# Kernel tuning notes

Measured on AMD Instinct MI355X. Metric: run time of the kernel, lower is better.

## Reference

```python
import jax, jax.numpy as jnp
import numpy as np

B, D_IN, D_HID, D_OUT, N_EXP, K = 32768, 256, 512, 256, 16, 2


def setup_inputs() -> dict:
    key = jax.random.key(0)
    ks = jax.random.split(key, 5)
    s_in = 1.0 / np.sqrt(D_IN)
    s_hid = 1.0 / np.sqrt(D_HID)
    return {
        "x": jax.random.normal(ks[0], (B, D_IN), jnp.float32),
        "Wg": jax.random.normal(ks[1], (D_IN, N_EXP), jnp.float32) * s_in,
        "bg": jnp.zeros((N_EXP,), jnp.float32),
        "W1": jax.random.normal(ks[2], (N_EXP, D_IN, D_HID), jnp.float32) * s_in,
        "b1": jnp.zeros((N_EXP, D_HID), jnp.float32),
        "W2": jax.random.normal(ks[3], (N_EXP, D_HID, D_OUT), jnp.float32) * s_hid,
        "b2": jnp.zeros((N_EXP, D_OUT), jnp.float32),
    }


def reference(x, Wg, bg, W1, b1, W2, b2):
    # Gating: linear -> softmax -> top-k -> renormalize (inference path, no noise)
    logits = x @ Wg + bg                       # [B, E]
    probs = jax.nn.softmax(logits, axis=-1)
    top_w, top_idx = jax.lax.top_k(probs, K)   # [B, K]
    top_w = top_w / jnp.sum(top_w, axis=-1, keepdims=True)

    # Expert MLPs (evaluate all experts densely, then gather selected outputs;
    # same math as masked gather -> MLP -> weighted scatter-add)
    h = jax.nn.relu(jnp.einsum('bi,eih->beh', x, W1) + b1[None])  # [B, E, H]
    y_all = jnp.einsum('beh,eho->beo', h, W2) + b2[None]          # [B, E, O]

    y_sel = jnp.take_along_axis(y_all, top_idx[:, :, None], axis=1)  # [B, K, O]
    return jnp.sum(y_sel * top_w[:, :, None], axis=1)                # [B, O]
```

## Files before the change

### kernel.cpp

```cpp
#include <hip/hip_runtime.h>
#include <stdint.h>

#define BTOK 32768
#define DIN 256
#define DHID 512
#define DOUT 256
#define NEXP 16
#define BM 128
#define CH 32
#define NCH 16
#define SLOTS 96

typedef __attribute__((ext_vector_type(8))) short bf16x8;
typedef __attribute__((ext_vector_type(4))) float f32x4;

__device__ __forceinline__ unsigned short f2bf(float f){
  unsigned u = __builtin_bit_cast(unsigned, f);
  u = u + 0x7FFFu + ((u >> 16) & 1u);
  return (unsigned short)(u >> 16);
}
__device__ __forceinline__ float bf2f(unsigned short h){
  return __builtin_bit_cast(float, (unsigned)h << 16);
}
__device__ __forceinline__ void gload16(const void* g, void* l){
  __builtin_amdgcn_global_load_lds((const __attribute__((address_space(1))) unsigned int*)g,
                                   (__attribute__((address_space(3))) unsigned int*)l, 16, 0, 0);
}

__global__ __launch_bounds__(256) void transpose_cvt(const float* __restrict__ src,
                                                     unsigned short* __restrict__ dst,
                                                     int R, int C){
  __shared__ float t[32][33];
  int e = blockIdx.z, r0 = blockIdx.y * 32, c0 = blockIdx.x * 32;
  int lx = threadIdx.x & 31, ly = threadIdx.x >> 5;
  const float* s = src + (size_t)e * R * C;
  unsigned short* d = dst + (size_t)e * R * C;
#pragma unroll
  for (int i = 0; i < 4; i++){ int r = ly + i * 8; t[r][lx] = s[(size_t)(r0 + r) * C + c0 + lx]; }
  __syncthreads();
#pragma unroll
  for (int i = 0; i < 4; i++){ int r = ly + i * 8; d[(size_t)(c0 + r) * R + r0 + lx] = f2bf(t[lx][r]); }
}

__global__ __launch_bounds__(256) void transpose_cvt_w2(const float* __restrict__ src,
                                                        unsigned short* __restrict__ dst){
  __shared__ float t[32][33];
  int e = blockIdx.z, r0 = blockIdx.y * 32, c0 = blockIdx.x * 32;
  int lx = threadIdx.x & 31, ly = threadIdx.x >> 5;
  const float* s = src + (size_t)e * DHID * DOUT;
  unsigned short* d = dst + (size_t)e * DHID * DOUT + (r0 >> 5) * (DOUT * CH);
#pragma unroll
  for (int i = 0; i < 4; i++){ int r = ly + i * 8; t[r][lx] = s[(size_t)(r0 + r) * DOUT + c0 + lx]; }
  __syncthreads();
#pragma unroll
  for (int i = 0; i < 4; i++){ int rr = ly + i * 8; d[(size_t)(c0 + rr) * CH + lx] = f2bf(t[lx][rr]); }
}

__global__ __launch_bounds__(256) void gating_kernel(const float* __restrict__ x,
                                                     const float* __restrict__ Wg,
                                                     const float* __restrict__ bg,
                                                     unsigned short* __restrict__ x_bf,
                                                     int* __restrict__ top_idx,
                                                     float* __restrict__ top_w,
                                                     int* __restrict__ counts){
  __shared__ float WgT[16][256];
  __shared__ int hist[16];
  int tid = threadIdx.x;
#pragma unroll
  for (int j = 0; j < 4; j++){
    float4 wv = *(const float4*)(Wg + tid * 16 + j * 4);
    WgT[j * 4 + 0][tid] = wv.x; WgT[j * 4 + 1][tid] = wv.y;
    WgT[j * 4 + 2][tid] = wv.z; WgT[j * 4 + 3][tid] = wv.w;
  }
  if (tid < 16) hist[tid] = 0;
  __syncthreads();
  int wid = tid >> 6, lane = tid & 63;

  for (int t = 0; t < 16; t++){
    int tok = blockIdx.x * 64 + wid * 16 + t;
    const float4 xv = *(const float4*)(x + (size_t)tok * DIN + lane * 4);
    ushort4 xb; xb.x = f2bf(xv.x); xb.y = f2bf(xv.y); xb.z = f2bf(xv.z); xb.w = f2bf(xv.w);
    *(ushort4*)(x_bf + (size_t)tok * DIN + lane * 4) = xb;
    float logit[16];
#pragma unroll
    for (int e = 0; e < 16; e++){
      const float4 wv = *(const float4*)(&WgT[e][lane * 4]);
      float v = xv.x * wv.x + xv.y * wv.y + xv.z * wv.z + xv.w * wv.w;
#pragma unroll
      for (int off = 32; off; off >>= 1) v += __shfl_xor(v, off, 64);
      logit[e] = v + bg[e];
    }
    if (lane == 0){
      int i1 = 0; float v1 = logit[0];
#pragma unroll
      for (int e = 1; e < 16; e++) if (logit[e] > v1){ v1 = logit[e]; i1 = e; }
      int i2 = -1; float v2 = -3.4e38f;
#pragma unroll
      for (int e = 0; e < 16; e++) if (e != i1 && logit[e] > v2){ v2 = logit[e]; i2 = e; }
      float tt = expf(v2 - v1);
      float w1 = 1.0f / (1.0f + tt);
      float w2 = tt / (1.0f + tt);
      top_idx[tok * 2] = i1; top_idx[tok * 2 + 1] = i2;
      top_w[tok * 2] = w1;  top_w[tok * 2 + 1] = w2;
      atomicAdd(&hist[i1], 1); atomicAdd(&hist[i2], 1);
    }
  }
  __syncthreads();
  if (tid < 16) atomicAdd(&counts[tid], hist[tid]);
}

__global__ void prefix_kernel(const int* __restrict__ counts, int* __restrict__ offsets,
                              int* __restrict__ cursor, int* __restrict__ bm_e,
                              int* __restrict__ bm_start, int* __restrict__ bm_end){
  int lane = threadIdx.x & 63;
  int c = (lane < 16) ? counts[lane] : 0;
  int s = c;
#pragma unroll
  for (int off = 1; off < 16; off <<= 1){ int o = __shfl_up(s, off, 64); if (lane >= off) s += o; }
  int start = s - c;
  if (lane < 16){ offsets[lane] = start; cursor[lane] = start; }
  int nb = (c + BM - 1) >> 7;
  int nb_partner = __shfl(nb, lane ^ 8, 64);
  if (lane < 8){
    int filled = nb + nb_partner;
    if (filled > SLOTS) filled = SLOTS;
    for (int i = filled; i < SLOTS; i++) bm_e[lane * SLOTS + i] = -1;
  }
  if (lane < 16){
    int sbase = (lane < 8) ? 0 : nb_partner;
    int xcd = lane & 7;
    for (int b = 0; b < nb; b++){
      int idx = xcd * SLOTS + sbase + b;
      if (sbase + b < SLOTS){
        bm_e[idx] = lane; bm_start[idx] = start + b * BM; bm_end[idx] = start + c;
      }
    }
  }
}

__global__ __launch_bounds__(256) void scatter_kernel(const int* __restrict__ top_idx,
                                                      const float* __restrict__ top_w,
                                                      int* __restrict__ cursor,
                                                      int* __restrict__ pair_tok,
                                                      float* __restrict__ pair_w,
                                                      int* __restrict__ pair_slot){
  __shared__ int hist[16], base[16], rank[16];
  int tid = threadIdx.x;
  if (tid < 16){ hist[tid] = 0; rank[tid] = 0; }
  __syncthreads();
  int t = blockIdx.x * 256 + tid;
  int e0 = top_idx[t * 2], e1 = top_idx[t * 2 + 1];
  float w0 = top_w[t * 2], w1 = top_w[t * 2 + 1];
  atomicAdd(&hist[e0], 1); atomicAdd(&hist[e1], 1);
  __syncthreads();
  if (tid < 16) base[tid] = atomicAdd(&cursor[tid], hist[tid]);
  __syncthreads();
  int r0 = atomicAdd(&rank[e0], 1);
  int p0 = base[e0] + r0;
  pair_tok[p0] = t; pair_w[p0] = w0; pair_slot[t * 2] = p0;
  int r1 = atomicAdd(&rank[e1], 1);
  int p1 = base[e1] + r1;
  pair_tok[p1] = t; pair_w[p1] = w1; pair_slot[t * 2 + 1] = p1;
}

__global__ __launch_bounds__(512, 1) void moe_gemm_kernel(
    const unsigned short* __restrict__ x_bf,
    const unsigned short* __restrict__ W1t,
    const unsigned short* __restrict__ W2c,
    const float* __restrict__ b1,
    const float* __restrict__ b2,
    const int* __restrict__ pair_tok, const float* __restrict__ pair_w,
    const int* __restrict__ bm_e, const int* __restrict__ bm_start,
    const int* __restrict__ bm_end,
    unsigned short* __restrict__ ypair){
  int xcd = blockIdx.x & 7, slot = blockIdx.x >> 3;
  int bmi = xcd * SLOTS + slot;
  int e = bm_e[bmi];
  if (e < 0) return;
  int rs = bm_start[bmi], re = bm_end[bmi];

  __shared__ unsigned short w1s[2][CH * 256];
  __shared__ unsigned short w2s[2][256 * CH];
  __shared__ unsigned short hs[BM * CH];
  __shared__ float b1s[DHID];
  char* hsb = (char*)hs;

  int tid = threadIdx.x, wid = tid >> 6, lane = tid & 63, lr = lane & 15, lh = lane >> 4;
  int mg = wid >> 1, ng = wid & 1;
  const char* gW1 = (const char*)(W1t + (size_t)e * DHID * DIN);
  const char* gW2 = (const char*)(W2c + (size_t)e * DOUT * DHID);

  b1s[tid] = b1[e * DHID + tid];

  int o1[2], o2[2];
#pragma unroll
  for (int k = 0; k < 2; k++){
    int g = k * 512 + tid;
    int r = g >> 5;
    o1[k] = r * 512 + ((g & 31) ^ (r & 7)) * 16;
    int p = g >> 3;
    int q = (g & 7) ^ (p & 7);
    int n = p * 2 + (q >> 2), sgr = q & 3;
    o2[k] = n * 64 + sgr * 16;
  }

  bf16x8 xr[2][8];
#pragma unroll
  for (int m = 0; m < 2; m++){
    int g0 = rs + 32 * mg + m * 16 + lr;
    int gc = g0 < re ? g0 : (re - 1);
    int tok = pair_tok[gc];
    const unsigned short* xrow = x_bf + (size_t)tok * DIN + lh * 8;
#pragma unroll
    for (int ks = 0; ks < 8; ks++) xr[m][ks] = *(const bf16x8*)(xrow + ks * 32);
  }

#define STAGE(c, sl) {                                                    \
    const char* s1 = gW1 + (size_t)(c) * 16384;                           \
    const char* s2 = gW2 + (size_t)(c) * 16384;                           \
    char* d1 = (char*)w1s[sl]; char* d2 = (char*)w2s[sl];                 \
    _Pragma("unroll")                                                     \
    for (int k = 0; k < 2; k++){                                          \
      gload16(s1 + o1[k], d1 + k * 8192 + wid * 1024);                    \
      gload16(s2 + o2[k], d2 + k * 8192 + wid * 1024);                    \
    } }

  f32x4 acc[2][8];
#pragma unroll
  for (int m = 0; m < 2; m++)
#pragma unroll
    for (int i = 0; i < 8; i++) acc[m][i] = (f32x4){0.f, 0.f, 0.f, 0.f};

  STAGE(0, 0);
  __syncthreads();

  for (int c = 0; c < NCH; c++){
    int sl = c & 1;
    if (c + 1 < NCH) STAGE(c + 1, sl ^ 1);

    const char* w1b = (const char*)w1s[sl];
    f32x4 hacc[2];
    hacc[0] = (f32x4){0.f, 0.f, 0.f, 0.f};
    hacc[1] = (f32x4){0.f, 0.f, 0.f, 0.f};
    int hrow = 16 * ng + lr;
#pragma unroll
    for (int ks = 0; ks < 8; ks++){
      bf16x8 b = *(const bf16x8*)(w1b + ((hrow * 512 + ks * 64 + lh * 16) ^ ((hrow & 7) << 4)));
      hacc[0] = __builtin_amdgcn_mfma_f32_16x16x32_bf16(xr[0][ks], b, hacc[0], 0, 0, 0);
      hacc[1] = __builtin_amdgcn_mfma_f32_16x16x32_bf16(xr[1][ks], b, hacc[1], 0, 0, 0);
    }

    {
      float b1v = b1s[c * CH + 16 * ng + lr];
      int col2 = (16 * ng + lr) * 2;
#pragma unroll
      for (int m = 0; m < 2; m++)
#pragma unroll
        for (int r = 0; r < 4; r++){
          int mm = 32 * mg + m * 16 + lh * 4 + r;
          float v = fmaxf(hacc[m][r] + b1v, 0.f);
          int adr = (mm >> 1) * 128 + ((((mm & 1) << 6) + col2) ^ (((mm >> 1) & 7) << 4));
          *(unsigned short*)(hsb + adr) = f2bf(v);
        }
    }
    __syncthreads();

    bf16x8 ha[2];
#pragma unroll
    for (int m = 0; m < 2; m++){
      int mm = 32 * mg + m * 16 + lr;
      int hadr = (mm >> 1) * 128 + ((((mm & 1) << 6) + (lh << 4)) ^ (((mm >> 1) & 7) << 4));
      ha[m] = *(const bf16x8*)(hsb + hadr);
    }
    const char* w2b = (const char*)w2s[sl];
#pragma unroll
    for (int nt = 0; nt < 8; nt++){
      int n = 128 * ng + nt * 16 + lr;
      int adr = (n >> 1) * 128 + ((((n & 1) << 6) + (lh << 4)) ^ (((n >> 1) & 7) << 4));
      bf16x8 b = *(const bf16x8*)(w2b + adr);
      acc[0][nt] = __builtin_amdgcn_mfma_f32_16x16x32_bf16(ha[0], b, acc[0][nt], 0, 0, 0);
      acc[1][nt] = __builtin_amdgcn_mfma_f32_16x16x32_bf16(ha[1], b, acc[1][nt], 0, 0, 0);
    }
    __syncthreads();
  }

#pragma unroll
  for (int m = 0; m < 2; m++){
    float wrow[4]; int grow[4];
#pragma unroll
    for (int r = 0; r < 4; r++){
      int gg = rs + 32 * mg + m * 16 + lh * 4 + r;
      grow[r] = gg;
      wrow[r] = (gg < re) ? pair_w[gg] : 0.f;
    }
#pragma unroll
    for (int nt = 0; nt < 8; nt++){
      int col = 128 * ng + nt * 16 + lr;
      float b2v = b2[e * DOUT + col];
#pragma unroll
      for (int r = 0; r < 4; r++){
        if (grow[r] < re)
          ypair[(size_t)grow[r] * DOUT + col] = f2bf(wrow[r] * (acc[m][nt][r] + b2v));
      }
    }
  }
#undef STAGE
}

__global__ __launch_bounds__(256) void combine_kernel(const unsigned short* __restrict__ yp,
                                                      const int* __restrict__ pair_slot,
                                                      float* __restrict__ out){
  int idx = blockIdx.x * 256 + threadIdx.x;
  int t = idx >> 6;
  int c4 = (idx & 63) << 2;
  int s0 = pair_slot[t * 2], s1 = pair_slot[t * 2 + 1];
  ushort4 a = *(const ushort4*)(yp + (size_t)s0 * DOUT + c4);
  ushort4 b = *(const ushort4*)(yp + (size_t)s1 * DOUT + c4);
  float4 o;
  o.x = bf2f(a.x) + bf2f(b.x);
  o.y = bf2f(a.y) + bf2f(b.y);
  o.z = bf2f(a.z) + bf2f(b.z);
  o.w = bf2f(a.w) + bf2f(b.w);
  *(float4*)(out + (size_t)t * DOUT + c4) = o;
}

extern "C" void kernel_launch(void* const* d_in, const int* in_sizes, int n_in,
                              void* d_out, int out_size, void* d_ws, size_t ws_size,
                              hipStream_t stream){
  (void)in_sizes; (void)n_in; (void)out_size; (void)ws_size;
  const float* x  = (const float*)d_in[0];
  const float* Wg = (const float*)d_in[1];
  const float* bg = (const float*)d_in[2];
  const float* W1 = (const float*)d_in[3];
  const float* b1 = (const float*)d_in[4];
  const float* W2 = (const float*)d_in[5];
  const float* b2 = (const float*)d_in[6];
  float* out = (float*)d_out;
  char* ws = (char*)d_ws;

  unsigned short* x_bf  = (unsigned short*)(ws);
  unsigned short* W1t   = (unsigned short*)(ws + 16777216);
  unsigned short* W2ck  = (unsigned short*)(ws + 20971520);
  unsigned short* ypair = (unsigned short*)(ws + 25165824);
  int*   top_idx  = (int*)  (ws + 58720256);
  float* top_w    = (float*)(ws + 58982400);
  int*   pair_tok = (int*)  (ws + 59244544);
  float* pair_w   = (float*)(ws + 59506688);
  int*   pair_slot= (int*)  (ws + 59768832);
  int*   counts   = (int*)  (ws + 60030976);
  int*   offsets  = (int*)  (ws + 60031040);
  int*   cursor   = (int*)  (ws + 60031104);
  int*   bm_e     = (int*)  (ws + 60031232);
  int*   bm_start = (int*)  (ws + 60036608);
  int*   bm_end   = (int*)  (ws + 60041984);

  hipMemsetAsync(counts, 0, 64, stream);
  transpose_cvt<<<dim3(16, 8, 16), 256, 0, stream>>>(W1, W1t, 256, 512);
  transpose_cvt_w2<<<dim3(8, 16, 16), 256, 0, stream>>>(W2, W2ck);
  gating_kernel<<<512, 256, 0, stream>>>(x, Wg, bg, x_bf, top_idx, top_w, counts);
  prefix_kernel<<<1, 64, 0, stream>>>(counts, offsets, cursor, bm_e, bm_start, bm_end);
  scatter_kernel<<<128, 256, 0, stream>>>(top_idx, top_w, cursor, pair_tok, pair_w, pair_slot);
  moe_gemm_kernel<<<8 * SLOTS, 512, 0, stream>>>(x_bf, W1t, W2ck, b1, b2, pair_tok, pair_w,
                                                 bm_e, bm_start, bm_end, ypair);
  combine_kernel<<<8192, 256, 0, stream>>>(ypair, pair_slot, out);
}
```

Before: 180.6 us.

## Halve expert row tile, read W2 from global, software-pipeline second GEMM

Shrinks the per-block row tile from 128 to 64 pairs and moves to 256-thread blocks with three blocks per CU, raising slot count accordingly. W2 is no longer staged through LDS and is loaded straight from global memory into registers. The hidden tile is double-buffered so the second GEMM for the previous chunk overlaps the first GEMM of the current chunk, with one barrier per chunk instead of two. This trades W1/W2 reuse per block and more global W2 traffic for higher occupancy and less LDS pressure and synchronisation.

```diff
diff --git a/kernel.cpp b/kernel.cpp
--- a/kernel.cpp
+++ b/kernel.cpp
@@ -6,10 +6,10 @@
 #define DHID 512
 #define DOUT 256
 #define NEXP 16
-#define BM 128
+#define BM 64
 #define CH 32
 #define NCH 16
-#define SLOTS 96
+#define SLOTS 168
 
 typedef __attribute__((ext_vector_type(8))) short bf16x8;
 typedef __attribute__((ext_vector_type(4))) float f32x4;
@@ -119,7 +119,7 @@
   for (int off = 1; off < 16; off <<= 1){ int o = __shfl_up(s, off, 64); if (lane >= off) s += o; }
   int start = s - c;
   if (lane < 16){ offsets[lane] = start; cursor[lane] = start; }
-  int nb = (c + BM - 1) >> 7;
+  int nb = (c + BM - 1) >> 6;
   int nb_partner = __shfl(nb, lane ^ 8, 64);
   if (lane < 8){
     int filled = nb + nb_partner;
@@ -163,7 +163,7 @@
   pair_tok[p1] = t; pair_w[p1] = w1; pair_slot[t * 2 + 1] = p1;
 }
 
-__global__ __launch_bounds__(512, 1) void moe_gemm_kernel(
+__global__ __launch_bounds__(256, 3) void moe_gemm_kernel(
     const unsigned short* __restrict__ x_bf,
     const unsigned short* __restrict__ W1t,
     const unsigned short* __restrict__ W2c,
@@ -180,10 +180,8 @@
   int rs = bm_start[bmi], re = bm_end[bmi];
 
   __shared__ unsigned short w1s[2][CH * 256];
-  __shared__ unsigned short w2s[2][256 * CH];
-  __shared__ unsigned short hs[BM * CH];
+  __shared__ unsigned short hs[2][BM * CH];
   __shared__ float b1s[DHID];
-  char* hsb = (char*)hs;
 
   int tid = threadIdx.x, wid = tid >> 6, lane = tid & 63, lr = lane & 15, lh = lane >> 4;
   int mg = wid >> 1, ng = wid & 1;
@@ -191,18 +189,9 @@
   const char* gW2 = (const char*)(W2c + (size_t)e * DOUT * DHID);
 
   b1s[tid] = b1[e * DHID + tid];
-
-  int o1[2], o2[2];
-#pragma unroll
-  for (int k = 0; k < 2; k++){
-    int g = k * 512 + tid;
-    int r = g >> 5;
-    o1[k] = r * 512 + ((g & 31) ^ (r & 7)) * 16;
-    int p = g >> 3;
-    int q = (g & 7) ^ (p & 7);
-    int n = p * 2 + (q >> 2), sgr = q & 3;
-    o2[k] = n * 64 + sgr * 16;
-  }
+  b1s[tid + 256] = b1[e * DHID + 256 + tid];
+
+  int o1 = ((tid >> 5) * 512) + (((tid & 31) ^ ((tid >> 5) & 7)) * 16);
 
   bf16x8 xr[2][8];
 #pragma unroll
@@ -217,13 +206,11 @@
 
 #define STAGE(c, sl) {                                                    \
     const char* s1 = gW1 + (size_t)(c) * 16384;                           \
-    const char* s2 = gW2 + (size_t)(c) * 16384;                           \
-    char* d1 = (char*)w1s[sl]; char* d2 = (char*)w2s[sl];                 \
+    char* d1 = (char*)w1s[sl];                                            \
     _Pragma("unroll")                                                     \
-    for (int k = 0; k < 2; k++){                                          \
-      gload16(s1 + o1[k], d1 + k * 8192 + wid * 1024);                    \
-      gload16(s2 + o2[k], d2 + k * 8192 + wid * 1024);                    \
-    } }
+    for (int k = 0; k < 4; k++)                                           \
+      gload16(s1 + o1 + k * 4096, d1 + tid * 16 + k * 4096);              \
+  }
 
   f32x4 acc[2][8];
 #pragma unroll
@@ -238,19 +225,38 @@
     int sl = c & 1;
     if (c + 1 < NCH) STAGE(c + 1, sl ^ 1);
 
-    const char* w1b = (const char*)w1s[sl];
-    f32x4 hacc[2];
-    hacc[0] = (f32x4){0.f, 0.f, 0.f, 0.f};
-    hacc[1] = (f32x4){0.f, 0.f, 0.f, 0.f};
-    int hrow = 16 * ng + lr;
-#pragma unroll
-    for (int ks = 0; ks < 8; ks++){
-      bf16x8 b = *(const bf16x8*)(w1b + ((hrow * 512 + ks * 64 + lh * 16) ^ ((hrow & 7) << 4)));
-      hacc[0] = __builtin_amdgcn_mfma_f32_16x16x32_bf16(xr[0][ks], b, hacc[0], 0, 0, 0);
-      hacc[1] = __builtin_amdgcn_mfma_f32_16x16x32_bf16(xr[1][ks], b, hacc[1], 0, 0, 0);
+    if (c > 0){
+      int pc = c - 1, psl = pc & 1;
+      const char* hpb = (const char*)hs[psl];
+      bf16x8 ha[2];
+#pragma unroll
+      for (int m = 0; m < 2; m++){
+        int mm = 32 * mg + m * 16 + lr;
+        int hadr = (mm >> 1) * 128 + ((((mm & 1) << 6) + (lh << 4)) ^ (((mm >> 1) & 7) << 4));
+        ha[m] = *(const bf16x8*)(hpb + hadr);
+      }
+      const char* w2base = gW2 + (size_t)pc * 16384 + ng * 8192 + lr * 64 + lh * 16;
+#pragma unroll
+      for (int nt = 0; nt < 8; nt++){
+        bf16x8 b = *(const bf16x8*)(w2base + nt * 1024);
+        acc[0][nt] = __builtin_amdgcn_mfma_f32_16x16x32_bf16(ha[0], b, acc[0][nt], 0, 0, 0);
+        acc[1][nt] = __builtin_amdgcn_mfma_f32_16x16x32_bf16(ha[1], b, acc[1][nt], 0, 0, 0);
+      }
     }
 
     {
+      const char* w1b = (const char*)w1s[sl];
+      f32x4 hacc[2];
+      hacc[0] = (f32x4){0.f, 0.f, 0.f, 0.f};
+      hacc[1] = (f32x4){0.f, 0.f, 0.f, 0.f};
+      int hrow = 16 * ng + lr;
+#pragma unroll
+      for (int ks = 0; ks < 8; ks++){
+        bf16x8 b = *(const bf16x8*)(w1b + ((hrow * 512 + ks * 64 + lh * 16) ^ ((hrow & 7) << 4)));
+        hacc[0] = __builtin_amdgcn_mfma_f32_16x16x32_bf16(xr[0][ks], b, hacc[0], 0, 0, 0);
+        hacc[1] = __builtin_amdgcn_mfma_f32_16x16x32_bf16(xr[1][ks], b, hacc[1], 0, 0, 0);
+      }
+      char* hwb = (char*)hs[sl];
       float b1v = b1s[c * CH + 16 * ng + lr];
       int col2 = (16 * ng + lr) * 2;
 #pragma unroll
@@ -260,28 +266,29 @@
           int mm = 32 * mg + m * 16 + lh * 4 + r;
           float v = fmaxf(hacc[m][r] + b1v, 0.f);
           int adr = (mm >> 1) * 128 + ((((mm & 1) << 6) + col2) ^ (((mm >> 1) & 7) << 4));
-          *(unsigned short*)(hsb + adr) = f2bf(v);
+          *(unsigned short*)(hwb + adr) = f2bf(v);
         }
     }
     __syncthreads();
-
+  }
+
+  {
+    int pc = NCH - 1, psl = pc & 1;
+    const char* hpb = (const char*)hs[psl];
     bf16x8 ha[2];
 #pragma unroll
     for (int m = 0; m < 2; m++){
       int mm = 32 * mg + m * 16 + lr;
       int hadr = (mm >> 1) * 128 + ((((mm & 1) << 6) + (lh << 4)) ^ (((mm >> 1) & 7) << 4));
-      ha[m] = *(const bf16x8*)(hsb + hadr);
-    }
-    const char* w2b = (const char*)w2s[sl];
+      ha[m] = *(const bf16x8*)(hpb + hadr);
+    }
+    const char* w2base = gW2 + (size_t)pc * 16384 + ng * 8192 + lr * 64 + lh * 16;
 #pragma unroll
     for (int nt = 0; nt < 8; nt++){
-      int n = 128 * ng + nt * 16 + lr;
-      int adr = (n >> 1) * 128 + ((((n & 1) << 6) + (lh << 4)) ^ (((n >> 1) & 7) << 4));
-      bf16x8 b = *(const bf16x8*)(w2b + adr);
+      bf16x8 b = *(const bf16x8*)(w2base + nt * 1024);
       acc[0][nt] = __builtin_amdgcn_mfma_f32_16x16x32_bf16(ha[0], b, acc[0][nt], 0, 0, 0);
       acc[1][nt] = __builtin_amdgcn_mfma_f32_16x16x32_bf16(ha[1], b, acc[1][nt], 0, 0, 0);
     }
-    __syncthreads();
   }
 
 #pragma unroll
@@ -360,7 +367,7 @@
   gating_kernel<<<512, 256, 0, stream>>>(x, Wg, bg, x_bf, top_idx, top_w, counts);
   prefix_kernel<<<1, 64, 0, stream>>>(counts, offsets, cursor, bm_e, bm_start, bm_end);
   scatter_kernel<<<128, 256, 0, stream>>>(top_idx, top_w, cursor, pair_tok, pair_w, pair_slot);
-  moe_gemm_kernel<<<8 * SLOTS, 512, 0, stream>>>(x_bf, W1t, W2ck, b1, b2, pair_tok, pair_w,
+  moe_gemm_kernel<<<8 * SLOTS, 256, 0, stream>>>(x_bf, W1t, W2ck, b1, b2, pair_tok, pair_w,
                                                  bm_e, bm_start, bm_end, ypair);
   combine_kernel<<<8192, 256, 0, stream>>>(ypair, pair_slot, out);
 }
```

Measured after the change: 217.2 us. +20.3%, slower.

## Triple-buffer weight staging with fine-grained waits and write ypair in token order

Applied to the files above, without the earlier changes.

The expert GEMM moves from a double-buffered to a triple-buffered LDS pipeline that prefetches two chunks ahead. The full __syncthreads barriers become raw s_barrier calls with partial vmcnt waits, so global loads can remain in flight across iterations. Separately, the slot index of each token is packed into pair_tok, so the GEMM epilogue writes ypair rows at token*2+k. This lets the combine kernel read contiguous rows and drops the pair_slot array. The cost is more LDS use and hand-written waitcnt logic that must exactly match the number of outstanding loads.

```diff
diff --git a/kernel.cpp b/kernel.cpp
--- a/kernel.cpp
+++ b/kernel.cpp
@@ -142,8 +142,7 @@
                                                       const float* __restrict__ top_w,
                                                       int* __restrict__ cursor,
                                                       int* __restrict__ pair_tok,
-                                                      float* __restrict__ pair_w,
-                                                      int* __restrict__ pair_slot){
+                                                      float* __restrict__ pair_w){
   __shared__ int hist[16], base[16], rank[16];
   int tid = threadIdx.x;
   if (tid < 16){ hist[tid] = 0; rank[tid] = 0; }
@@ -157,10 +156,10 @@
   __syncthreads();
   int r0 = atomicAdd(&rank[e0], 1);
   int p0 = base[e0] + r0;
-  pair_tok[p0] = t; pair_w[p0] = w0; pair_slot[t * 2] = p0;
+  pair_tok[p0] = t; pair_w[p0] = w0;
   int r1 = atomicAdd(&rank[e1], 1);
   int p1 = base[e1] + r1;
-  pair_tok[p1] = t; pair_w[p1] = w1; pair_slot[t * 2 + 1] = p1;
+  pair_tok[p1] = t | (1 << 16); pair_w[p1] = w1;
 }
 
 __global__ __launch_bounds__(512, 1) void moe_gemm_kernel(
@@ -179,51 +178,44 @@
   if (e < 0) return;
   int rs = bm_start[bmi], re = bm_end[bmi];
 
-  __shared__ unsigned short w1s[2][CH * 256];
-  __shared__ unsigned short w2s[2][256 * CH];
+  __shared__ unsigned short w1s[3][CH * 256];
+  __shared__ unsigned short w2s[3][256 * CH];
   __shared__ unsigned short hs[BM * CH];
   __shared__ float b1s[DHID];
-  char* hsb = (char*)hs;
 
   int tid = threadIdx.x, wid = tid >> 6, lane = tid & 63, lr = lane & 15, lh = lane >> 4;
   int mg = wid >> 1, ng = wid & 1;
+  char* hsb = (char*)hs;
   const char* gW1 = (const char*)(W1t + (size_t)e * DHID * DIN);
   const char* gW2 = (const char*)(W2c + (size_t)e * DOUT * DHID);
 
   b1s[tid] = b1[e * DHID + tid];
 
-  int o1[2], o2[2];
-#pragma unroll
-  for (int k = 0; k < 2; k++){
-    int g = k * 512 + tid;
-    int r = g >> 5;
-    o1[k] = r * 512 + ((g & 31) ^ (r & 7)) * 16;
-    int p = g >> 3;
-    int q = (g & 7) ^ (p & 7);
-    int n = p * 2 + (q >> 2), sgr = q & 3;
-    o2[k] = n * 64 + sgr * 16;
-  }
-
-  bf16x8 xr[2][8];
-#pragma unroll
-  for (int m = 0; m < 2; m++){
-    int g0 = rs + 32 * mg + m * 16 + lr;
-    int gc = g0 < re ? g0 : (re - 1);
-    int tok = pair_tok[gc];
-    const unsigned short* xrow = x_bf + (size_t)tok * DIN + lh * 8;
-#pragma unroll
-    for (int ks = 0; ks < 8; ks++) xr[m][ks] = *(const bf16x8*)(xrow + ks * 32);
-  }
+  int o1 = ((tid >> 5) * 512) + (((tid & 31) ^ ((tid >> 5) & 7)) * 16);
+  int o2;
+  { int p = tid >> 3, q = (tid & 7) ^ (p & 7);
+    o2 = (p * 2 + (q >> 2)) * 64 + (q & 3) * 16; }
 
 #define STAGE(c, sl) {                                                    \
     const char* s1 = gW1 + (size_t)(c) * 16384;                           \
     const char* s2 = gW2 + (size_t)(c) * 16384;                           \
     char* d1 = (char*)w1s[sl]; char* d2 = (char*)w2s[sl];                 \
-    _Pragma("unroll")                                                     \
-    for (int k = 0; k < 2; k++){                                          \
-      gload16(s1 + o1[k], d1 + k * 8192 + wid * 1024);                    \
-      gload16(s2 + o2[k], d2 + k * 8192 + wid * 1024);                    \
-    } }
+    gload16(s1 + o1,        d1 + tid * 16);                               \
+    gload16(s1 + o1 + 8192, d1 + tid * 16 + 8192);                        \
+    gload16(s2 + o2,        d2 + tid * 16);                               \
+    gload16(s2 + o2 + 8192, d2 + tid * 16 + 8192);                        \
+  }
+
+  bf16x8 xr[2][8];
+#pragma unroll
+  for (int m = 0; m < 2; m++){
+    int g0 = rs + 32 * mg + m * 16 + lr;
+    int gc = g0 < re ? g0 : (re - 1);
+    int tok = pair_tok[gc] & 0xFFFF;
+    const unsigned short* xrow = x_bf + (size_t)tok * DIN + lh * 8;
+#pragma unroll
+    for (int ks = 0; ks < 8; ks++) xr[m][ks] = *(const bf16x8*)(xrow + ks * 32);
+  }
 
   f32x4 acc[2][8];
 #pragma unroll
@@ -231,26 +223,26 @@
 #pragma unroll
     for (int i = 0; i < 8; i++) acc[m][i] = (f32x4){0.f, 0.f, 0.f, 0.f};
 
-  STAGE(0, 0);
-  __syncthreads();
-
+  STAGE(0, 0); STAGE(1, 1);
+  __syncthreads();
+
+#pragma unroll 1
   for (int c = 0; c < NCH; c++){
-    int sl = c & 1;
-    if (c + 1 < NCH) STAGE(c + 1, sl ^ 1);
-
-    const char* w1b = (const char*)w1s[sl];
-    f32x4 hacc[2];
-    hacc[0] = (f32x4){0.f, 0.f, 0.f, 0.f};
-    hacc[1] = (f32x4){0.f, 0.f, 0.f, 0.f};
-    int hrow = 16 * ng + lr;
-#pragma unroll
-    for (int ks = 0; ks < 8; ks++){
-      bf16x8 b = *(const bf16x8*)(w1b + ((hrow * 512 + ks * 64 + lh * 16) ^ ((hrow & 7) << 4)));
-      hacc[0] = __builtin_amdgcn_mfma_f32_16x16x32_bf16(xr[0][ks], b, hacc[0], 0, 0, 0);
-      hacc[1] = __builtin_amdgcn_mfma_f32_16x16x32_bf16(xr[1][ks], b, hacc[1], 0, 0, 0);
-    }
+    int b0 = c % 3;
+    if (c + 2 < NCH) STAGE(c + 2, (c + 2) % 3);
 
     {
+      const char* w1b = (const char*)w1s[b0];
+      f32x4 hacc[2];
+      hacc[0] = (f32x4){0.f, 0.f, 0.f, 0.f};
+      hacc[1] = (f32x4){0.f, 0.f, 0.f, 0.f};
+      int hrow = 16 * ng + lr;
+#pragma unroll
+      for (int ks = 0; ks < 8; ks++){
+        bf16x8 b = *(const bf16x8*)(w1b + ((hrow * 512 + ks * 64 + lh * 16) ^ ((hrow & 7) << 4)));
+        hacc[0] = __builtin_amdgcn_mfma_f32_16x16x32_bf16(xr[0][ks], b, hacc[0], 0, 0, 0);
+        hacc[1] = __builtin_amdgcn_mfma_f32_16x16x32_bf16(xr[1][ks], b, hacc[1], 0, 0, 0);
+      }
       float b1v = b1s[c * CH + 16 * ng + lr];
       int col2 = (16 * ng + lr) * 2;
 #pragma unroll
@@ -263,35 +255,52 @@
           *(unsigned short*)(hsb + adr) = f2bf(v);
         }
     }
-    __syncthreads();
-
-    bf16x8 ha[2];
-#pragma unroll
-    for (int m = 0; m < 2; m++){
-      int mm = 32 * mg + m * 16 + lr;
-      int hadr = (mm >> 1) * 128 + ((((mm & 1) << 6) + (lh << 4)) ^ (((mm >> 1) & 7) << 4));
-      ha[m] = *(const bf16x8*)(hsb + hadr);
-    }
-    const char* w2b = (const char*)w2s[sl];
-#pragma unroll
-    for (int nt = 0; nt < 8; nt++){
-      int n = 128 * ng + nt * 16 + lr;
-      int adr = (n >> 1) * 128 + ((((n & 1) << 6) + (lh << 4)) ^ (((n >> 1) & 7) << 4));
-      bf16x8 b = *(const bf16x8*)(w2b + adr);
-      acc[0][nt] = __builtin_amdgcn_mfma_f32_16x16x32_bf16(ha[0], b, acc[0][nt], 0, 0, 0);
-      acc[1][nt] = __builtin_amdgcn_mfma_f32_16x16x32_bf16(ha[1], b, acc[1][nt], 0, 0, 0);
-    }
-    __syncthreads();
+    asm volatile("s_waitcnt lgkmcnt(0)" ::: "memory");
+    __builtin_amdgcn_sched_barrier(0);
+    __builtin_amdgcn_s_barrier();
+    __builtin_amdgcn_sched_barrier(0);
+
+    {
+      const char* w2b = (const char*)w2s[b0];
+      bf16x8 ha[2];
+#pragma unroll
+      for (int m = 0; m < 2; m++){
+        int mm = 32 * mg + m * 16 + lr;
+        int hadr = (mm >> 1) * 128 + ((((mm & 1) << 6) + (lh << 4)) ^ (((mm >> 1) & 7) << 4));
+        ha[m] = *(const bf16x8*)(hsb + hadr);
+      }
+#pragma unroll
+      for (int nt = 0; nt < 8; nt++){
+        int n = 128 * ng + nt * 16 + lr;
+        int adr = (n >> 1) * 128 + ((((n & 1) << 6) + (lh << 4)) ^ (((n >> 1) & 7) << 4));
+        bf16x8 b = *(const bf16x8*)(w2b + adr);
+        acc[0][nt] = __builtin_amdgcn_mfma_f32_16x16x32_bf16(ha[0], b, acc[0][nt], 0, 0, 0);
+        acc[1][nt] = __builtin_amdgcn_mfma_f32_16x16x32_bf16(ha[1], b, acc[1][nt], 0, 0, 0);
+      }
+    }
+    if (c + 1 < NCH){
+      if (c + 2 < NCH){
+        asm volatile("s_waitcnt vmcnt(4) lgkmcnt(0)" ::: "memory");
+      } else {
+        asm volatile("s_waitcnt vmcnt(0) lgkmcnt(0)" ::: "memory");
+      }
+      __builtin_amdgcn_sched_barrier(0);
+      __builtin_amdgcn_s_barrier();
+      __builtin_amdgcn_sched_barrier(0);
+    }
   }
 
 #pragma unroll
   for (int m = 0; m < 2; m++){
-    float wrow[4]; int grow[4];
+    float wrow[4]; int yrow[4]; int valid[4];
 #pragma unroll
     for (int r = 0; r < 4; r++){
       int gg = rs + 32 * mg + m * 16 + lh * 4 + r;
-      grow[r] = gg;
-      wrow[r] = (gg < re) ? pair_w[gg] : 0.f;
+      valid[r] = gg < re;
+      int gc = valid[r] ? gg : (re - 1);
+      int pt = pair_tok[gc];
+      yrow[r] = (pt & 0xFFFF) * 2 + (pt >> 16);
+      wrow[r] = valid[r] ? pair_w[gc] : 0.f;
     }
 #pragma unroll
     for (int nt = 0; nt < 8; nt++){
@@ -299,8 +308,8 @@
       float b2v = b2[e * DOUT + col];
 #pragma unroll
       for (int r = 0; r < 4; r++){
-        if (grow[r] < re)
-          ypair[(size_t)grow[r] * DOUT + col] = f2bf(wrow[r] * (acc[m][nt][r] + b2v));
+        if (valid[r])
+          ypair[(size_t)yrow[r] * DOUT + col] = f2bf(wrow[r] * (acc[m][nt][r] + b2v));
       }
     }
   }
@@ -308,14 +317,12 @@
 }
 
 __global__ __launch_bounds__(256) void combine_kernel(const unsigned short* __restrict__ yp,
-                                                      const int* __restrict__ pair_slot,
                                                       float* __restrict__ out){
   int idx = blockIdx.x * 256 + threadIdx.x;
   int t = idx >> 6;
   int c4 = (idx & 63) << 2;
-  int s0 = pair_slot[t * 2], s1 = pair_slot[t * 2 + 1];
-  ushort4 a = *(const ushort4*)(yp + (size_t)s0 * DOUT + c4);
-  ushort4 b = *(const ushort4*)(yp + (size_t)s1 * DOUT + c4);
+  ushort4 a = *(const ushort4*)(yp + (size_t)(t * 2) * DOUT + c4);
+  ushort4 b = *(const ushort4*)(yp + (size_t)(t * 2 + 1) * DOUT + c4);
   float4 o;
   o.x = bf2f(a.x) + bf2f(b.x);
   o.y = bf2f(a.y) + bf2f(b.y);
@@ -346,7 +353,6 @@
   float* top_w    = (float*)(ws + 58982400);
   int*   pair_tok = (int*)  (ws + 59244544);
   float* pair_w   = (float*)(ws + 59506688);
-  int*   pair_slot= (int*)  (ws + 59768832);
   int*   counts   = (int*)  (ws + 60030976);
   int*   offsets  = (int*)  (ws + 60031040);
   int*   cursor   = (int*)  (ws + 60031104);
@@ -359,8 +365,8 @@
   transpose_cvt_w2<<<dim3(8, 16, 16), 256, 0, stream>>>(W2, W2ck);
   gating_kernel<<<512, 256, 0, stream>>>(x, Wg, bg, x_bf, top_idx, top_w, counts);
   prefix_kernel<<<1, 64, 0, stream>>>(counts, offsets, cursor, bm_e, bm_start, bm_end);
-  scatter_kernel<<<128, 256, 0, stream>>>(top_idx, top_w, cursor, pair_tok, pair_w, pair_slot);
+  scatter_kernel<<<128, 256, 0, stream>>>(top_idx, top_w, cursor, pair_tok, pair_w);
   moe_gemm_kernel<<<8 * SLOTS, 512, 0, stream>>>(x_bf, W1t, W2ck, b1, b2, pair_tok, pair_w,
                                                  bm_e, bm_start, bm_end, ypair);
-  combine_kernel<<<8192, 256, 0, stream>>>(ypair, pair_slot, out);
-}
+  combine_kernel<<<8192, 256, 0, stream>>>(ypair, out);
+}
```

Result: faster. 174.2 us (-3.6%).
